# Performance work log

Hardware: AMD Instinct MI355X
Metric: run time of the kernel (lower is better)

The kernel has to match this reference:

```python
import jax, jax.numpy as jnp
import numpy as np

B, S, DIM = 64, 576, 768
KEEP_TOKEN = 64  # module keeps KEEP_TOKEN-1 top patches + 1 pooled extra token
HID = 128       # autoencoder bottleneck


def setup_inputs() -> dict:
    key = jax.random.key(0)
    k1, k2, k3, k4 = jax.random.split(key, 4)
    cls_emb = jax.random.normal(k1, (B, DIM), dtype=jnp.float32)
    fm = jax.random.normal(k2, (B, S, DIM), dtype=jnp.float32)
    # autoencoder: Linear(dim,128) -> Tanh -> Linear(128,dim); y = x @ W + b
    W1 = jax.random.normal(k3, (DIM, HID), dtype=jnp.float32) / np.sqrt(DIM)
    b1 = jnp.zeros((HID,), dtype=jnp.float32)
    W2 = jax.random.normal(k4, (HID, DIM), dtype=jnp.float32) / np.sqrt(HID)
    b2 = jnp.zeros((DIM,), dtype=jnp.float32)
    return {"cls_emb": cls_emb, "fm": fm, "W1": W1, "b1": b1, "W2": W2, "b2": b2}


def reference(cls_emb, fm, W1, b1, W2, b2):
    # cls attention scores over patch tokens: [B, S]
    cls_attn = jnp.einsum('bd,bsd->bs', cls_emb, fm)
    # top-(K-1) patches by cls attention (largest, sorted)
    _, idx = jax.lax.top_k(cls_attn, KEEP_TOKEN - 1)           # [B, K-1]
    top_token = jnp.take_along_axis(fm, idx[:, :, None], axis=1)  # [B, K-1, DIM]
    # mask selected positions (one_hot(idx).sum(1) -> 0/1 since topk idx unique)
    batch_ix = jnp.arange(fm.shape[0])[:, None]
    one_hot_idx = jnp.zeros_like(cls_attn).at[batch_ix, idx].add(1.0)  # [B, S]
    weight = jax.nn.softmax(one_hot_idx * -10000.0 + cls_attn, axis=1)[:, :, None]
    extra_token = jnp.sum(weight * fm, axis=1, keepdims=True)  # [B, 1, DIM]
    visual_tokens = jnp.concatenate([top_token, extra_token], axis=1)  # [B, K, DIM]
    ae = lambda x: jnp.tanh(x @ W1 + b1) @ W2 + b2
    return ae(visual_tokens), ae(cls_emb)
```

## Files before the change

### kernel.cpp

```cpp
#include <hip/hip_runtime.h>
#include <math.h>

#define BB   64
#define SS   576
#define DD   768
#define KTOP 63
#define KEEP 64
#define HH   128
#define NROW (BB*KEEP + BB)
#define SCH  24

typedef unsigned long long ull;

__global__ __launch_bounds__(256) void k_scores(const float* __restrict__ cls,
                                                const float* __restrict__ fm,
                                                float* __restrict__ scores)
{
  int gw = (blockIdx.x * blockDim.x + threadIdx.x) >> 6;
  int lane = threadIdx.x & 63;
  if (gw >= BB * SS) return;
  int b = gw / SS, s = gw - b * SS;
  const float4* frow = (const float4*)(fm + ((size_t)b * SS + s) * DD);
  const float4* crow = (const float4*)(cls + (size_t)b * DD);
  double acc = 0.0;
#pragma unroll
  for (int j = 0; j < 3; ++j) {
    float4 f = frow[lane + 64 * j];
    float4 c = crow[lane + 64 * j];
    acc += (double)f.x * c.x + (double)f.y * c.y + (double)f.z * c.z + (double)f.w * c.w;
  }
#pragma unroll
  for (int off = 32; off > 0; off >>= 1) acc += __shfl_down(acc, off, 64);
  if (lane == 0) scores[(size_t)b * SS + s] = (float)acc;
}

__global__ __launch_bounds__(576) void k_rank(const float* __restrict__ scores,
                                              int* __restrict__ idxout,
                                              int* __restrict__ cidx,
                                              float* __restrict__ cw,
                                              int* __restrict__ ccount)
{
  __shared__ ull keys[SS];
  __shared__ float redm[9], redz[9];
  __shared__ unsigned wcnt[9];
  int b = blockIdx.x, tid = threadIdx.x;
  int lane = tid & 63, wid = tid >> 6;
  float sc = scores[(size_t)b * SS + tid];
  unsigned int u = __float_as_uint(sc);
  u = (u & 0x80000000u) ? ~u : (u | 0x80000000u);
  ull key = ((ull)u << 32) | (ull)(0xFFFFFFFFu - (unsigned)tid);
  keys[tid] = key;
  __syncthreads();
  int rank = 0;
#pragma unroll 8
  for (int s = 0; s < SS; ++s) rank += (keys[s] > key) ? 1 : 0;
  bool sel = rank < KTOP;
  if (sel) idxout[b * KEEP + rank] = tid;
  float m = sel ? -1e30f : sc;
#pragma unroll
  for (int off = 32; off; off >>= 1) m = fmaxf(m, __shfl_xor(m, off, 64));
  if (lane == 0) redm[wid] = m;
  __syncthreads();
  float M = redm[0];
#pragma unroll
  for (int i = 1; i < 9; ++i) M = fmaxf(M, redm[i]);
  float e = sel ? 0.f : expf(sc - M);
  float z = e;
#pragma unroll
  for (int off = 32; off; off >>= 1) z += __shfl_xor(z, off, 64);
  if (lane == 0) redz[wid] = z;
  __syncthreads();
  float Z = redz[0];
#pragma unroll
  for (int i = 1; i < 9; ++i) Z += redz[i];
  float w = e / Z;
  bool keep = w > 1e-10f;
  ull ball = __ballot(keep);
  int wpre = __popcll(ball & ((1ull << lane) - 1ull));
  if (lane == 0) wcnt[wid] = (unsigned)__popcll(ball);
  __syncthreads();
  int base = 0;
#pragma unroll
  for (int i = 0; i < 9; ++i) base += (i < wid) ? (int)wcnt[i] : 0;
  if (keep) {
    int pos = base + wpre;
    cidx[(size_t)b * SS + pos] = tid;
    cw[(size_t)b * SS + pos] = w;
  }
  if (tid == 0) {
    int tot = 0;
#pragma unroll
    for (int i = 0; i < 9; ++i) tot += (int)wcnt[i];
    ccount[b] = tot;
  }
}

__global__ __launch_bounds__(192) void k_extra2(const int* __restrict__ cidx,
                                                const float* __restrict__ cw,
                                                const int* __restrict__ ccount,
                                                const float* __restrict__ fm,
                                                float* __restrict__ epart)
{
  int b = blockIdx.x, p = blockIdx.y, tid = threadIdx.x;
  int n = ccount[b];
  const float* fb = fm + (size_t)b * SS * DD + tid * 4;
  float4 acc = make_float4(0.f, 0.f, 0.f, 0.f);
  for (int r = p; r < n; r += SCH) {
    float w = cw[(size_t)b * SS + r];
    int s = cidx[(size_t)b * SS + r];
    float4 v = *(const float4*)(fb + (size_t)s * DD);
    acc.x = fmaf(w, v.x, acc.x); acc.y = fmaf(w, v.y, acc.y);
    acc.z = fmaf(w, v.z, acc.z); acc.w = fmaf(w, v.w, acc.w);
  }
  *(float4*)(epart + (size_t)(b * SCH + p) * DD + tid * 4) = acc;
}

template<int CPB>
__global__ __launch_bounds__(256, 3) void k_ae1(const float* __restrict__ fm,
                                                const float* __restrict__ cls,
                                                const float* __restrict__ epart,
                                                const int* __restrict__ idxin,
                                                const float* __restrict__ W1,
                                                float* __restrict__ partial)
{
  __shared__ float Xs[64][68];
  __shared__ float Ws[64][132];
  __shared__ const float* rowptr[64];
  int g = blockIdx.x;
  int tid = threadIdx.x;
  bool batch = (g < BB);

  if (tid < 64) {
    const float* p;
    if (batch) {
      p = (tid < KTOP) ? fm + ((size_t)g * SS + idxin[g * KEEP + tid]) * DD
                       : epart + (size_t)(g * SCH) * DD;
    } else {
      p = cls + (size_t)tid * DD;
    }
    rowptr[tid] = p;
  }

  int ty = tid >> 5, tx = tid & 31;
  int r0 = ty * 8, c0 = tx * 4;
  float acc[8][4] = {};

  for (int cc = 0; cc < CPB; ++cc) {
    int kb = (blockIdx.y * CPB + cc) * 64;
    __syncthreads();
#pragma unroll
    for (int i = 0; i < 4; ++i) {
      int f4 = tid + 256 * i;
      int r = f4 >> 4, k4 = f4 & 15;
      if (!batch || r != 63)
        *(float4*)&Xs[r][k4 * 4] = *(const float4*)(rowptr[r] + kb + k4 * 4);
    }
    if (batch && tid < 16) {
      float4 s = make_float4(0.f, 0.f, 0.f, 0.f);
#pragma unroll
      for (int p = 0; p < SCH; ++p) {
        float4 t = *(const float4*)(epart + (size_t)(g * SCH + p) * DD + kb + tid * 4);
        s.x += t.x; s.y += t.y; s.z += t.z; s.w += t.w;
      }
      *(float4*)&Xs[63][tid * 4] = s;
    }
#pragma unroll
    for (int i = 0; i < 8; ++i) {
      int f4 = tid + 256 * i;
      int wr = f4 >> 5, c4 = f4 & 31;
      *(float4*)&Ws[wr][c4 * 4] =
          *(const float4*)(W1 + (size_t)(kb + wr) * HH + c4 * 4);
    }
    __syncthreads();
#pragma unroll
    for (int q = 0; q < 16; ++q) {
      float4 xv[8], wv[4];
#pragma unroll
      for (int i = 0; i < 8; ++i) xv[i] = *(const float4*)&Xs[r0 + i][q * 4];
#pragma unroll
      for (int j = 0; j < 4; ++j) wv[j] = *(const float4*)&Ws[q * 4 + j][c0];
#pragma unroll
      for (int i = 0; i < 8; ++i) {
        float x;
        x = xv[i].x;
        acc[i][0] = fmaf(x, wv[0].x, acc[i][0]); acc[i][1] = fmaf(x, wv[0].y, acc[i][1]);
        acc[i][2] = fmaf(x, wv[0].z, acc[i][2]); acc[i][3] = fmaf(x, wv[0].w, acc[i][3]);
        x = xv[i].y;
        acc[i][0] = fmaf(x, wv[1].x, acc[i][0]); acc[i][1] = fmaf(x, wv[1].y, acc[i][1]);
        acc[i][2] = fmaf(x, wv[1].z, acc[i][2]); acc[i][3] = fmaf(x, wv[1].w, acc[i][3]);
        x = xv[i].z;
        acc[i][0] = fmaf(x, wv[2].x, acc[i][0]); acc[i][1] = fmaf(x, wv[2].y, acc[i][1]);
        acc[i][2] = fmaf(x, wv[2].z, acc[i][2]); acc[i][3] = fmaf(x, wv[2].w, acc[i][3]);
        x = xv[i].w;
        acc[i][0] = fmaf(x, wv[3].x, acc[i][0]); acc[i][1] = fmaf(x, wv[3].y, acc[i][1]);
        acc[i][2] = fmaf(x, wv[3].z, acc[i][2]); acc[i][3] = fmaf(x, wv[3].w, acc[i][3]);
      }
    }
  }
  float* P = partial + (size_t)(CPB == 1 ? blockIdx.y : 0) * ((size_t)NROW * HH);
#pragma unroll
  for (int i = 0; i < 8; ++i) {
    float4 v = make_float4(acc[i][0], acc[i][1], acc[i][2], acc[i][3]);
    *(float4*)&P[(size_t)(g * 64 + r0 + i) * HH + c0] = v;
  }
}

template<int NP>
__global__ __launch_bounds__(256) void k_hred(const float* __restrict__ partial,
                                              const float* __restrict__ b1,
                                              float* __restrict__ H)
{
  int i4 = blockIdx.x * 256 + threadIdx.x;
  const float4* P = (const float4*)partial;
  float4 s = P[i4];
#pragma unroll
  for (int p = 1; p < NP; ++p) {
    float4 t = P[(size_t)p * (NROW * HH / 4) + i4];
    s.x += t.x; s.y += t.y; s.z += t.z; s.w += t.w;
  }
  float4 bv = ((const float4*)b1)[i4 & 31];
  s.x = tanhf(s.x + bv.x); s.y = tanhf(s.y + bv.y);
  s.z = tanhf(s.z + bv.z); s.w = tanhf(s.w + bv.w);
  ((float4*)H)[i4] = s;
}

__global__ __launch_bounds__(256, 2) void k_ae2(const float* __restrict__ H,
                                                const float* __restrict__ W2,
                                                const float* __restrict__ b2,
                                                float* __restrict__ out)
{
  __shared__ float Hs[64][132];
  __shared__ float Ws[128][68];
  int g = blockIdx.x;
  int cb = blockIdx.y;
  int tid = threadIdx.x;

#pragma unroll
  for (int i = 0; i < 8; ++i) {
    int f4 = tid + 256 * i;
    int r = f4 >> 5, c4 = f4 & 31;
    *(float4*)&Hs[r][c4 * 4] = *(const float4*)(H + (size_t)(g * 64 + r) * HH + c4 * 4);
  }
#pragma unroll
  for (int i = 0; i < 8; ++i) {
    int f4 = tid + 256 * i;
    int wr = f4 >> 4, c4 = f4 & 15;
    *(float4*)&Ws[wr][c4 * 4] =
        *(const float4*)(W2 + (size_t)wr * DD + cb * 64 + c4 * 4);
  }
  __syncthreads();

  int ty = tid >> 4, tx = tid & 15;
  int r0 = ty * 4, c0 = tx * 4;
  float acc[4][4] = {};
#pragma unroll 4
  for (int q = 0; q < 32; ++q) {
    float4 xv[4], wv[4];
#pragma unroll
    for (int i = 0; i < 4; ++i) xv[i] = *(const float4*)&Hs[r0 + i][q * 4];
#pragma unroll
    for (int j = 0; j < 4; ++j) wv[j] = *(const float4*)&Ws[q * 4 + j][c0];
#pragma unroll
    for (int i = 0; i < 4; ++i) {
      float x;
      x = xv[i].x;
      acc[i][0] = fmaf(x, wv[0].x, acc[i][0]); acc[i][1] = fmaf(x, wv[0].y, acc[i][1]);
      acc[i][2] = fmaf(x, wv[0].z, acc[i][2]); acc[i][3] = fmaf(x, wv[0].w, acc[i][3]);
      x = xv[i].y;
      acc[i][0] = fmaf(x, wv[1].x, acc[i][0]); acc[i][1] = fmaf(x, wv[1].y, acc[i][1]);
      acc[i][2] = fmaf(x, wv[1].z, acc[i][2]); acc[i][3] = fmaf(x, wv[1].w, acc[i][3]);
      x = xv[i].z;
      acc[i][0] = fmaf(x, wv[2].x, acc[i][0]); acc[i][1] = fmaf(x, wv[2].y, acc[i][1]);
      acc[i][2] = fmaf(x, wv[2].z, acc[i][2]); acc[i][3] = fmaf(x, wv[2].w, acc[i][3]);
      x = xv[i].w;
      acc[i][0] = fmaf(x, wv[3].x, acc[i][0]); acc[i][1] = fmaf(x, wv[3].y, acc[i][1]);
      acc[i][2] = fmaf(x, wv[3].z, acc[i][2]); acc[i][3] = fmaf(x, wv[3].w, acc[i][3]);
    }
  }
  float4 bv = *(const float4*)&b2[cb * 64 + c0];
#pragma unroll
  for (int i = 0; i < 4; ++i) {
    float4 y = make_float4(acc[i][0] + bv.x, acc[i][1] + bv.y,
                           acc[i][2] + bv.z, acc[i][3] + bv.w);
    *(float4*)&out[(size_t)(g * 64 + r0 + i) * DD + cb * 64 + c0] = y;
  }
}

extern "C" void kernel_launch(void* const* d_in, const int* in_sizes, int n_in,
                              void* d_out, int out_size, void* d_ws, size_t ws_size,
                              hipStream_t stream)
{
  const float* cls = (const float*)d_in[0];
  const float* fm  = (const float*)d_in[1];
  const float* W1  = (const float*)d_in[2];
  const float* b1  = (const float*)d_in[3];
  const float* W2  = (const float*)d_in[4];
  const float* b2  = (const float*)d_in[5];
  float* out = (float*)d_out;

  char* ws = (char*)d_ws;
  float* scores  = (float*)ws;
  int*   idx     = (int*)(ws + 147456);
  int*   cidx    = (int*)(ws + 163840);
  float* cw      = (float*)(ws + 311296);
  int*   ccount  = (int*)(ws + 458752);
  float* epart   = (float*)(ws + 459776);
  float* partial = (float*)(ws + 5178368);
  const size_t PSLICE = (size_t)NROW * HH * 4;

  hipLaunchKernelGGL(k_scores, dim3((BB * SS) / 4), dim3(256), 0, stream, cls, fm, scores);
  hipLaunchKernelGGL(k_rank,   dim3(BB),            dim3(576), 0, stream,
                     scores, idx, cidx, cw, ccount);
  hipLaunchKernelGGL(k_extra2, dim3(BB, SCH),       dim3(192), 0, stream,
                     cidx, cw, ccount, fm, epart);

  if (ws_size >= 5178368 + 13 * PSLICE) {
    float* H = (float*)(ws + 5178368 + 12 * PSLICE);
    hipLaunchKernelGGL(k_ae1<1>,  dim3(65, 12),      dim3(256), 0, stream,
                       fm, cls, epart, idx, W1, partial);
    hipLaunchKernelGGL(k_hred<12>, dim3(NROW * HH / 1024), dim3(256), 0, stream,
                       partial, b1, H);
    hipLaunchKernelGGL(k_ae2,     dim3(65, 12),      dim3(256), 0, stream, H, W2, b2, out);
  } else {
    float* H = (float*)(ws + 5178368 + PSLICE);
    hipLaunchKernelGGL(k_ae1<12>, dim3(65, 1),       dim3(256), 0, stream,
                       fm, cls, epart, idx, W1, partial);
    hipLaunchKernelGGL(k_hred<1>, dim3(NROW * HH / 1024), dim3(256), 0, stream,
                       partial, b1, H);
    hipLaunchKernelGGL(k_ae2,     dim3(65, 12),      dim3(256), 0, stream, H, W2, b2, out);
  }
}
```

Before: 89.97 us.

## Fuse extra-token weighted sum into the first autoencoder GEMM kernel

Removes the separate k_extra2 kernel and its epart partial-sum buffer. Each k_ae1 block for a batch now computes the softmax-weighted sum over the compacted candidate rows for its 64-column chunk directly into the shared-memory row 63, using 64 threads and cross-lane shuffle reduction. This saves a kernel launch and the write and reread of partial sums, but it puts a serial, latency-bound gather loop over up to hundreds of rows on only 64 threads inside the GEMM block, which may stall the other threads at the barrier.

```diff
diff --git a/kernel.cpp b/kernel.cpp
--- a/kernel.cpp
+++ b/kernel.cpp
@@ -8,7 +8,6 @@
 #define KEEP 64
 #define HH   128
 #define NROW (BB*KEEP + BB)
-#define SCH  24
 
 typedef unsigned long long ull;
 
@@ -95,30 +94,12 @@
   }
 }
 
-__global__ __launch_bounds__(192) void k_extra2(const int* __restrict__ cidx,
-                                                const float* __restrict__ cw,
-                                                const int* __restrict__ ccount,
-                                                const float* __restrict__ fm,
-                                                float* __restrict__ epart)
-{
-  int b = blockIdx.x, p = blockIdx.y, tid = threadIdx.x;
-  int n = ccount[b];
-  const float* fb = fm + (size_t)b * SS * DD + tid * 4;
-  float4 acc = make_float4(0.f, 0.f, 0.f, 0.f);
-  for (int r = p; r < n; r += SCH) {
-    float w = cw[(size_t)b * SS + r];
-    int s = cidx[(size_t)b * SS + r];
-    float4 v = *(const float4*)(fb + (size_t)s * DD);
-    acc.x = fmaf(w, v.x, acc.x); acc.y = fmaf(w, v.y, acc.y);
-    acc.z = fmaf(w, v.z, acc.z); acc.w = fmaf(w, v.w, acc.w);
-  }
-  *(float4*)(epart + (size_t)(b * SCH + p) * DD + tid * 4) = acc;
-}
-
 template<int CPB>
 __global__ __launch_bounds__(256, 3) void k_ae1(const float* __restrict__ fm,
                                                 const float* __restrict__ cls,
-                                                const float* __restrict__ epart,
+                                                const int* __restrict__ cidx,
+                                                const float* __restrict__ cw,
+                                                const int* __restrict__ ccount,
                                                 const int* __restrict__ idxin,
                                                 const float* __restrict__ W1,
                                                 float* __restrict__ partial)
@@ -129,16 +110,12 @@
   int g = blockIdx.x;
   int tid = threadIdx.x;
   bool batch = (g < BB);
-
-  if (tid < 64) {
-    const float* p;
-    if (batch) {
-      p = (tid < KTOP) ? fm + ((size_t)g * SS + idxin[g * KEEP + tid]) * DD
-                       : epart + (size_t)(g * SCH) * DD;
-    } else {
-      p = cls + (size_t)tid * DD;
-    }
-    rowptr[tid] = p;
+  int n = batch ? ccount[g] : 0;
+
+  if (tid < 63 && batch) {
+    rowptr[tid] = fm + ((size_t)g * SS + idxin[g * KEEP + tid]) * DD;
+  } else if (tid < 64 && !batch) {
+    rowptr[tid] = cls + (size_t)tid * DD;
   }
 
   int ty = tid >> 5, tx = tid & 31;
@@ -155,14 +132,23 @@
       if (!batch || r != 63)
         *(float4*)&Xs[r][k4 * 4] = *(const float4*)(rowptr[r] + kb + k4 * 4);
     }
-    if (batch && tid < 16) {
-      float4 s = make_float4(0.f, 0.f, 0.f, 0.f);
-#pragma unroll
-      for (int p = 0; p < SCH; ++p) {
-        float4 t = *(const float4*)(epart + (size_t)(g * SCH + p) * DD + kb + tid * 4);
-        s.x += t.x; s.y += t.y; s.z += t.z; s.w += t.w;
+    if (batch && tid < 64) {
+      int c4 = tid & 15, sub = tid >> 4;
+      const float* fb = fm + (size_t)g * SS * DD + kb + c4 * 4;
+      const int* ci = cidx + (size_t)g * SS;
+      const float* cwp = cw + (size_t)g * SS;
+      float4 a = make_float4(0.f, 0.f, 0.f, 0.f);
+      for (int r = sub; r < n; r += 4) {
+        float w = cwp[r];
+        float4 v = *(const float4*)(fb + (size_t)ci[r] * DD);
+        a.x = fmaf(w, v.x, a.x); a.y = fmaf(w, v.y, a.y);
+        a.z = fmaf(w, v.z, a.z); a.w = fmaf(w, v.w, a.w);
       }
-      *(float4*)&Xs[63][tid * 4] = s;
+      a.x += __shfl_xor(a.x, 16); a.y += __shfl_xor(a.y, 16);
+      a.z += __shfl_xor(a.z, 16); a.w += __shfl_xor(a.w, 16);
+      a.x += __shfl_xor(a.x, 32); a.y += __shfl_xor(a.y, 32);
+      a.z += __shfl_xor(a.z, 32); a.w += __shfl_xor(a.w, 32);
+      if (sub == 0) *(float4*)&Xs[63][c4 * 4] = a;
     }
 #pragma unroll
     for (int i = 0; i < 8; ++i) {
@@ -304,27 +290,24 @@
   int*   cidx    = (int*)(ws + 163840);
   float* cw      = (float*)(ws + 311296);
   int*   ccount  = (int*)(ws + 458752);
-  float* epart   = (float*)(ws + 459776);
-  float* partial = (float*)(ws + 5178368);
+  float* partial = (float*)(ws + 459776);
   const size_t PSLICE = (size_t)NROW * HH * 4;
 
   hipLaunchKernelGGL(k_scores, dim3((BB * SS) / 4), dim3(256), 0, stream, cls, fm, scores);
   hipLaunchKernelGGL(k_rank,   dim3(BB),            dim3(576), 0, stream,
                      scores, idx, cidx, cw, ccount);
-  hipLaunchKernelGGL(k_extra2, dim3(BB, SCH),       dim3(192), 0, stream,
-                     cidx, cw, ccount, fm, epart);
-
-  if (ws_size >= 5178368 + 13 * PSLICE) {
-    float* H = (float*)(ws + 5178368 + 12 * PSLICE);
+
+  if (ws_size >= 459776 + 13 * PSLICE) {
+    float* H = (float*)(ws + 459776 + 12 * PSLICE);
     hipLaunchKernelGGL(k_ae1<1>,  dim3(65, 12),      dim3(256), 0, stream,
-                       fm, cls, epart, idx, W1, partial);
+                       fm, cls, cidx, cw, ccount, idx, W1, partial);
     hipLaunchKernelGGL(k_hred<12>, dim3(NROW * HH / 1024), dim3(256), 0, stream,
                        partial, b1, H);
     hipLaunchKernelGGL(k_ae2,     dim3(65, 12),      dim3(256), 0, stream, H, W2, b2, out);
   } else {
-    float* H = (float*)(ws + 5178368 + PSLICE);
+    float* H = (float*)(ws + 459776 + PSLICE);
     hipLaunchKernelGGL(k_ae1<12>, dim3(65, 1),       dim3(256), 0, stream,
-                       fm, cls, epart, idx, W1, partial);
+                       fm, cls, cidx, cw, ccount, idx, W1, partial);
     hipLaunchKernelGGL(k_hred<1>, dim3(NROW * HH / 1024), dim3(256), 0, stream,
                        partial, b1, H);
     hipLaunchKernelGGL(k_ae2,     dim3(65, 12),      dim3(256), 0, stream, H, W2, b2, out);
```

After: 98.75 us. +9.8%, slower.

## Fuse split-K reduction and tanh into ae1 via last-block atomic counter

Applied to the files above, without the earlier changes.

Removes the separate k_hred kernel. Each ae1 block now increments a per-row-group atomic counter after writing its partial result, and the last block to finish sums all split-K partials, adds the bias, applies tanh and writes H. The counters are zeroed in k_rank. This saves one kernel launch and its extra pass over memory, at the cost of a threadfence, an atomic, and a serial reduction tail that runs on one block per group.

```diff
diff --git a/kernel.cpp b/kernel.cpp
--- a/kernel.cpp
+++ b/kernel.cpp
@@ -38,13 +38,16 @@
                                               int* __restrict__ idxout,
                                               int* __restrict__ cidx,
                                               float* __restrict__ cw,
-                                              int* __restrict__ ccount)
+                                              int* __restrict__ ccount,
+                                              int* __restrict__ cnt)
 {
   __shared__ ull keys[SS];
   __shared__ float redm[9], redz[9];
   __shared__ unsigned wcnt[9];
   int b = blockIdx.x, tid = threadIdx.x;
   int lane = tid & 63, wid = tid >> 6;
+  if (tid == 0) cnt[b] = 0;
+  if (b == 0 && tid == 1) cnt[64] = 0;
   float sc = scores[(size_t)b * SS + tid];
   unsigned int u = __float_as_uint(sc);
   u = (u & 0x80000000u) ? ~u : (u | 0x80000000u);
@@ -115,17 +118,21 @@
   *(float4*)(epart + (size_t)(b * SCH + p) * DD + tid * 4) = acc;
 }
 
-template<int CPB>
+template<int CPB, int NB>
 __global__ __launch_bounds__(256, 3) void k_ae1(const float* __restrict__ fm,
                                                 const float* __restrict__ cls,
                                                 const float* __restrict__ epart,
                                                 const int* __restrict__ idxin,
                                                 const float* __restrict__ W1,
-                                                float* __restrict__ partial)
+                                                const float* __restrict__ b1,
+                                                float* __restrict__ partial,
+                                                float* __restrict__ H,
+                                                int* __restrict__ cnt)
 {
   __shared__ float Xs[64][68];
   __shared__ float Ws[64][132];
   __shared__ const float* rowptr[64];
+  __shared__ int lastflag;
   int g = blockIdx.x;
   int tid = threadIdx.x;
   bool batch = (g < BB);
@@ -203,25 +210,32 @@
     float4 v = make_float4(acc[i][0], acc[i][1], acc[i][2], acc[i][3]);
     *(float4*)&P[(size_t)(g * 64 + r0 + i) * HH + c0] = v;
   }
-}
-
-template<int NP>
-__global__ __launch_bounds__(256) void k_hred(const float* __restrict__ partial,
-                                              const float* __restrict__ b1,
-                                              float* __restrict__ H)
-{
-  int i4 = blockIdx.x * 256 + threadIdx.x;
-  const float4* P = (const float4*)partial;
-  float4 s = P[i4];
-#pragma unroll
-  for (int p = 1; p < NP; ++p) {
-    float4 t = P[(size_t)p * (NROW * HH / 4) + i4];
-    s.x += t.x; s.y += t.y; s.z += t.z; s.w += t.w;
-  }
-  float4 bv = ((const float4*)b1)[i4 & 31];
-  s.x = tanhf(s.x + bv.x); s.y = tanhf(s.y + bv.y);
-  s.z = tanhf(s.z + bv.z); s.w = tanhf(s.w + bv.w);
-  ((float4*)H)[i4] = s;
+
+  __threadfence();
+  if (tid == 0) {
+    int prev = (NB > 1) ? atomicAdd(&cnt[g], 1) : (NB - 1);
+    lastflag = (prev == NB - 1) ? 1 : 0;
+  }
+  __syncthreads();
+  if (lastflag) {
+    __threadfence();
+#pragma unroll
+    for (int i = 0; i < 8; ++i) {
+      int f4 = tid + 256 * i;
+      int r = f4 >> 5, c4 = f4 & 31;
+      size_t off = (size_t)(g * 64 + r) * HH + c4 * 4;
+      float4 s = *(const float4*)&partial[off];
+#pragma unroll
+      for (int p = 1; p < NB; ++p) {
+        float4 t = *(const float4*)&partial[(size_t)p * ((size_t)NROW * HH) + off];
+        s.x += t.x; s.y += t.y; s.z += t.z; s.w += t.w;
+      }
+      float4 bv = *(const float4*)&b1[c4 * 4];
+      s.x = tanhf(s.x + bv.x); s.y = tanhf(s.y + bv.y);
+      s.z = tanhf(s.z + bv.z); s.w = tanhf(s.w + bv.w);
+      *(float4*)&H[off] = s;
+    }
+  }
 }
 
 __global__ __launch_bounds__(256, 2) void k_ae2(const float* __restrict__ H,
@@ -304,29 +318,26 @@
   int*   cidx    = (int*)(ws + 163840);
   float* cw      = (float*)(ws + 311296);
   int*   ccount  = (int*)(ws + 458752);
+  int*   cnt     = (int*)(ws + 459008);
   float* epart   = (float*)(ws + 459776);
   float* partial = (float*)(ws + 5178368);
   const size_t PSLICE = (size_t)NROW * HH * 4;
 
   hipLaunchKernelGGL(k_scores, dim3((BB * SS) / 4), dim3(256), 0, stream, cls, fm, scores);
   hipLaunchKernelGGL(k_rank,   dim3(BB),            dim3(576), 0, stream,
-                     scores, idx, cidx, cw, ccount);
+                     scores, idx, cidx, cw, ccount, cnt);
   hipLaunchKernelGGL(k_extra2, dim3(BB, SCH),       dim3(192), 0, stream,
                      cidx, cw, ccount, fm, epart);
 
   if (ws_size >= 5178368 + 13 * PSLICE) {
     float* H = (float*)(ws + 5178368 + 12 * PSLICE);
-    hipLaunchKernelGGL(k_ae1<1>,  dim3(65, 12),      dim3(256), 0, stream,
-                       fm, cls, epart, idx, W1, partial);
-    hipLaunchKernelGGL(k_hred<12>, dim3(NROW * HH / 1024), dim3(256), 0, stream,
-                       partial, b1, H);
-    hipLaunchKernelGGL(k_ae2,     dim3(65, 12),      dim3(256), 0, stream, H, W2, b2, out);
+    hipLaunchKernelGGL((k_ae1<1, 12>), dim3(65, 12),  dim3(256), 0, stream,
+                       fm, cls, epart, idx, W1, b1, partial, H, cnt);
+    hipLaunchKernelGGL(k_ae2,          dim3(65, 12),  dim3(256), 0, stream, H, W2, b2, out);
   } else {
     float* H = (float*)(ws + 5178368 + PSLICE);
-    hipLaunchKernelGGL(k_ae1<12>, dim3(65, 1),       dim3(256), 0, stream,
-                       fm, cls, epart, idx, W1, partial);
-    hipLaunchKernelGGL(k_hred<1>, dim3(NROW * HH / 1024), dim3(256), 0, stream,
-                       partial, b1, H);
-    hipLaunchKernelGGL(k_ae2,     dim3(65, 12),      dim3(256), 0, stream, H, W2, b2, out);
-  }
-}
+    hipLaunchKernelGGL((k_ae1<12, 1>), dim3(65, 1),   dim3(256), 0, stream,
+                       fm, cls, epart, idx, W1, b1, partial, H, cnt);
+    hipLaunchKernelGGL(k_ae2,          dim3(65, 12),  dim3(256), 0, stream, H, W2, b2, out);
+  }
+}
```

Measured after the change: 185.3 us. 2.06x slower.
